# Performance work log

Measured on AMD Instinct MI355X. Metric: run time of the kernel, lower is better.

Reference implementation:

```python
import jax, jax.numpy as jnp
import numpy as np

H, DM, LQ, LK, DK, DV = 16, 1024, 2048, 2048, 64, 64
B = 2

def setup_inputs() -> dict:
    key = jax.random.key(0)
    ks = jax.random.split(key, 12)
    s = 0.02  # init scale for weights
    return {
        "Q": jax.random.normal(ks[0], (B, LQ, DM), jnp.float32),
        "K": jax.random.normal(ks[1], (B, LK, DM), jnp.float32),
        "V": jax.random.normal(ks[2], (B, LK, DM), jnp.float32),
        "mask": jax.random.randint(ks[3], (B, LQ), 0, 2, jnp.int32),
        "W_Q": jax.random.normal(ks[4], (H * DK, DM), jnp.float32) * s,
        "b_Q": jnp.zeros((H * DK,), jnp.float32),
        "W_K": jax.random.normal(ks[5], (H * DK, DM), jnp.float32) * s,
        "b_K": jnp.zeros((H * DK,), jnp.float32),
        "W_V": jax.random.normal(ks[6], (H * DV, DM), jnp.float32) * s,
        "b_V": jnp.zeros((H * DV,), jnp.float32),
        "W_O": jax.random.normal(ks[7], (DM, H * DV), jnp.float32) * s,
        "b_O": jnp.zeros((DM,), jnp.float32),
    }

def reference(Q, K, V, mask, W_Q, b_Q, W_K, b_K, W_V, b_V, W_O, b_O):
    b = Q.shape[0]
    q = (Q @ W_Q.T + b_Q).reshape(b, LQ, H, DK)
    k = (K @ W_K.T + b_K).reshape(b, LK, H, DK)
    v = (V @ W_V.T + b_V).reshape(b, LK, H, DV)
    # scores: [b, h, q, k]
    A = jnp.einsum('bqhd,bkhd->bhqk', q, k) / jnp.sqrt(jnp.float32(DK))
    # mask masks whole QUERY rows; softmax is over the query axis (dim=1 in torch's [B*h, lq, lk])
    A = jnp.where(mask[:, None, :, None] == 0, -jnp.inf, A)
    alpha = jax.nn.softmax(A, axis=2)  # over query axis, per original masked branch
    out = jnp.einsum('bhqk,bkhd->bqhd', alpha, v).reshape(b, LQ, H * DV)
    return out @ W_O.T + b_O + Q  # output proj + residual
```

## Files before the change

### kernel.cpp

```cpp
#include <hip/hip_runtime.h>
#include <hip/hip_bf16.h>
#include <stdint.h>

using frag8 = __attribute__((ext_vector_type(8))) short;
using f32x4 = __attribute__((ext_vector_type(4))) float;

#define MFMA16 __builtin_amdgcn_mfma_f32_16x16x32_bf16

#if __has_builtin(__builtin_amdgcn_exp2f)
#define EXP2F(x) __builtin_amdgcn_exp2f(x)
#else
#define EXP2F(x) __expf((x) * 0.6931471805599453f)
#endif
#if __has_builtin(__builtin_amdgcn_rcpf)
#define RCPF(x) __builtin_amdgcn_rcpf(x)
#else
#define RCPF(x) (1.0f / (x))
#endif

#define SCALE_Q 0.18033688011112042f

__device__ __forceinline__ short f2bf(float f) {
    union { __hip_bfloat16 h; short s; } c;
    c.h = __float2bfloat16(f);
    return c.s;
}
__device__ __forceinline__ float bf2f(short s) {
    union { uint32_t u; float f; } x; x.u = ((uint32_t)(uint16_t)s) << 16;
    return x.f;
}
__device__ __forceinline__ uint32_t pack2bf(float a, float b) {
    float2 t; t.x = a; t.y = b;
    __hip_bfloat162 h = __float22bfloat162_rn(t);
    union { __hip_bfloat162 h; uint32_t u; } c; c.h = h;
    return c.u;
}
__device__ __forceinline__ uint32_t addpk(uint32_t a, uint32_t b) {
    float a0 = bf2f((short)(a & 0xffff)), a1 = bf2f((short)(a >> 16));
    float b0 = bf2f((short)(b & 0xffff)), b1 = bf2f((short)(b >> 16));
    return pack2bf(a0 + b0, a1 + b1);
}
__device__ __forceinline__ frag8 add8(uint4 x, uint4 y) {
    union { uint32_t u[4]; frag8 f; } r;
    r.u[0] = addpk(x.x, y.x); r.u[1] = addpk(x.y, y.y);
    r.u[2] = addpk(x.z, y.z); r.u[3] = addpk(x.w, y.w);
    return r.f;
}

__global__ __launch_bounds__(64) void k_compact(const int* __restrict__ mask,
                                                int* __restrict__ idx,
                                                int* __restrict__ invp,
                                                int* __restrict__ nU) {
    const int b = blockIdx.x, ln = threadIdx.x;
    const int* m = mask + b * 2048;
    int tot = 0;
    for (int c = 0; c < 32; c++)
        tot += __popcll(__ballot(m[c * 64 + ln] != 0));
    int base = 0, mbase = tot;
    for (int c = 0; c < 32; c++) {
        int i = c * 64 + ln;
        int mv = m[i];
        unsigned long long bal = __ballot(mv != 0);
        int rank = __popcll(bal & ((1ull << ln) - 1ull));
        int nb = __popcll(bal);
        int pos = mv ? (base + rank) : (mbase + ln - rank);
        invp[b * 2048 + i] = pos;
        if (mv) idx[b * 2048 + pos] = i;
        base += nb; mbase += 64 - nb;
    }
    if (ln == 0) nU[b] = tot;
}

__global__ __launch_bounds__(256) void k_psum(short* __restrict__ p0,
                                              const short* __restrict__ p1, int n8) {
    int i = blockIdx.x * 256 + threadIdx.x;
    int st = gridDim.x * 256;
    for (; i < n8; i += st) {
        uint4 a = ((const uint4*)p0)[i];
        uint4 b = ((const uint4*)p1)[i];
        frag8 r = add8(a, b);
        ((uint4*)p0)[i] = *(uint4*)&r;
    }
}

__global__ __launch_bounds__(256) void k_maskout(const int* __restrict__ mask,
                                                 const float* __restrict__ bO,
                                                 const float* __restrict__ Qf,
                                                 float* __restrict__ out) {
    int i = blockIdx.x * 256 + threadIdx.x;
    int st = gridDim.x * 256;
    const int total = 4096 * 256;
    for (; i < total; i += st) {
        int row = i >> 8, c4 = i & 255;
        if (mask[row] == 0) {
            float4 q = ((const float4*)Qf)[i];
            float4 bv = ((const float4*)bO)[c4];
            float4 o; o.x = q.x + bv.x; o.y = q.y + bv.y;
            o.z = q.z + bv.z; o.w = q.w + bv.w;
            ((float4*)out)[i] = o;
        }
    }
}

__global__ __launch_bounds__(256) void k_cvt_all(
    const float* __restrict__ s0, const float* __restrict__ s1,
    const float* __restrict__ s2, const float* __restrict__ s3,
    const float* __restrict__ s4, const float* __restrict__ s5,
    const float* __restrict__ s6, const int* __restrict__ invp,
    short* __restrict__ d0, short* __restrict__ d1, short* __restrict__ d2,
    short* __restrict__ d3, short* __restrict__ d4, short* __restrict__ d5,
    short* __restrict__ d6) {
    const int A4 = 1048576, W4 = 262144;
    int i = blockIdx.x * 256 + threadIdx.x;
    int st = gridDim.x * 256;
    const int total = 3 * A4 + 4 * W4;
    for (; i < total; i += st) {
        const float* s; short* d; int j;
        bool permQ = false;
        if (i < A4)            { s = s0; d = d0; j = i; permQ = true; }
        else if (i < 2 * A4)   { s = s1; d = d1; j = i - A4; }
        else if (i < 3 * A4)   { s = s2; d = d2; j = i - 2 * A4; }
        else {
            int t = i - 3 * A4; int seg = t / W4; j = t - seg * W4;
            s = seg == 0 ? s3 : seg == 1 ? s4 : seg == 2 ? s5 : s6;
            d = seg == 0 ? d3 : seg == 1 ? d4 : seg == 2 ? d5 : d6;
        }
        float4 v = reinterpret_cast<const float4*>(s)[j];
        uint2 o;
        o.x = pack2bf(v.x, v.y);
        o.y = pack2bf(v.z, v.w);
        int jd = j;
        if (permQ) {
            int row = j >> 8, c4 = j & 255;
            int nrow = (row & ~2047) + invp[row];
            jd = (nrow << 8) + c4;
        }
        reinterpret_cast<uint2*>(d)[jd] = o;
    }
}

__device__ __forceinline__ void stage64x128(const short* __restrict__ g, int rs,
                                            short* lds, int tid) {
#pragma unroll
    for (int j = 0; j < 2; j++) {
        int chunk = j * 256 + tid;
        int row = chunk >> 3, c = chunk & 7;
        int sc = c ^ (row & 7);
        __builtin_amdgcn_global_load_lds(
            (const __attribute__((address_space(1))) uint32_t*)(g + (size_t)row * rs + sc * 8),
            (__attribute__((address_space(3))) uint32_t*)(lds + (j * 256 + (tid & 192)) * 8),
            16, 0, 0);
    }
}
__device__ __forceinline__ frag8 ldswz(const short* lds, int row, int cc) {
    return *(const frag8*)(lds + row * 64 + ((cc ^ (row & 7)) << 3));
}

__device__ __forceinline__ void stage_gswz(const short* __restrict__ g,
                                           short* lds, int tid) {
#pragma unroll
    for (int j = 0; j < 2; j++) {
        int c = j * 256 + tid;
        int lrow = c >> 3;
        int sc = (c & 7) ^ (lrow & 7);
        int grow = lrow * 2 + (sc >> 2);
        int gcol = (sc & 3) * 8;
        __builtin_amdgcn_global_load_lds(
            (const __attribute__((address_space(1))) uint32_t*)(g + (size_t)grow * 1024 + gcol),
            (__attribute__((address_space(3))) uint32_t*)(lds + (j * 256 + (tid & 192)) * 8),
            16, 0, 0);
    }
}
__device__ __forceinline__ void stage_gswz64(const short* __restrict__ g,
                                             short* lds, int tid) {
    int c = tid;
    int lrow = c >> 3;
    int sc = (c & 7) ^ (lrow & 7);
    int grow = lrow * 2 + (sc >> 2);
    int gcol = (sc & 3) * 8;
    __builtin_amdgcn_global_load_lds(
        (const __attribute__((address_space(1))) uint32_t*)(g + (size_t)grow * 1024 + gcol),
        (__attribute__((address_space(3))) uint32_t*)(lds + (tid & 192) * 8),
        16, 0, 0);
}
__device__ __forceinline__ frag8 ldgswz(const short* lds, int row, int cc) {
    int lrow = row >> 1;
    int s = (((row & 1) << 2) + cc) ^ (lrow & 7);
    return *(const frag8*)(lds + lrow * 64 + s * 8);
}

__global__ __launch_bounds__(256) void k_proj3(
    const short* __restrict__ A0, const short* __restrict__ A1, const short* __restrict__ A2,
    const short* __restrict__ B0, const short* __restrict__ B1, const short* __restrict__ B2,
    const float* __restrict__ bias0, const float* __restrict__ bias1, const float* __restrict__ bias2,
    const int* __restrict__ nU,
    short* __restrict__ dst0, short* __restrict__ dst1, short* __restrict__ dst2) {
    __shared__ short lA[2][4096];
    __shared__ short lB[2][4096];
    const int wg = blockIdx.x;
    const int tmlow = wg & 7, tnb = (wg >> 3) & 7, rest = wg >> 6;
    const int tmh = rest & 3, z = rest >> 2;
    const int tmb = tmlow | (tmh << 3);
    if (z == 0 && (tmb & 15) * 128 >= nU[tmb >> 4]) return;
    const short* A  = z == 0 ? A0 : z == 1 ? A1 : A2;
    const short* Bt = z == 0 ? B0 : z == 1 ? B1 : B2;
    const float* bias = z == 0 ? bias0 : z == 1 ? bias1 : bias2;
    short* dst = z == 0 ? dst0 : z == 1 ? dst1 : dst2;
    const float scale = z == 0 ? SCALE_Q : 1.0f;

    const int tid = threadIdx.x, w = tid >> 6, ln = tid & 63;
    const int wm = w >> 1, wn = w & 1, r16 = ln & 15, g = ln >> 4;
    const int tn = tnb * 128, tm = tmb * 128;
    const short* Ab = A + (size_t)tm * 1024;
    const short* Bb = Bt + (size_t)tn * 1024;

    f32x4 acc[4][4] = {};
    stage_gswz(Ab, &lA[0][0], tid);
    stage_gswz(Bb, &lB[0][0], tid);
    int buf = 0;
    for (int ks = 0; ks < 32; ks++) {
        __syncthreads();
        if (ks + 1 < 32) {
            stage_gswz(Ab + (ks + 1) * 32, &lA[buf ^ 1][0], tid);
            stage_gswz(Bb + (ks + 1) * 32, &lB[buf ^ 1][0], tid);
        }
        frag8 af[4], bg[4];
#pragma unroll
        for (int mf = 0; mf < 4; mf++)
            af[mf] = ldgswz(&lA[buf][0], wm * 64 + mf * 16 + r16, g);
#pragma unroll
        for (int nf = 0; nf < 4; nf++)
            bg[nf] = ldgswz(&lB[buf][0], wn * 64 + nf * 16 + r16, g);
#pragma unroll
        for (int mf = 0; mf < 4; mf++)
#pragma unroll
            for (int nf = 0; nf < 4; nf++)
                acc[mf][nf] = MFMA16(af[mf], bg[nf], acc[mf][nf], 0, 0, 0);
        buf ^= 1;
    }
#pragma unroll
    for (int mf = 0; mf < 4; mf++)
#pragma unroll
        for (int r = 0; r < 4; r++) {
            int m = tm + wm * 64 + mf * 16 + g * 4 + r;
            int b = m >> 11, seq = m & 2047;
#pragma unroll
            for (int nf = 0; nf < 4; nf++) {
                int n = tn + wn * 64 + nf * 16 + r16;
                float val = (acc[mf][nf][r] + bias[n]) * scale;
                int h = n >> 6, d = n & 63;
                dst[((size_t)(b * 16 + h) * 2048 + seq) * 64 + d] = f2bf(val);
            }
        }
}

__global__ __launch_bounds__(256, 3) void k_stats(const short* __restrict__ k_s,
                                                  const short* __restrict__ q_s,
                                                  const int* __restrict__ nU,
                                                  const short* __restrict__ v_s,
                                                  short* __restrict__ vhatT) {
    __shared__ short lQ[2][4096];
    __shared__ float lD[128];
    __shared__ short lT[128 * 70];
    const int wg = blockIdx.x;
    const int x = wg & 7, r2 = wg >> 3;
    const int kt = r2 & 15;
    const int bh = x + 8 * (r2 >> 4);
    const int b = bh >> 4;
    const int n = nU[b], nUr = (n + 63) & ~63;
    const int tid = threadIdx.x, w = tid >> 6, ln = tid & 63;
    const int r16 = ln & 15, g = ln >> 4;
    const int kbase = kt * 128 + w * 32;

    const short* kp = k_s + ((size_t)bh * 2048 + kbase) * 64;
    frag8 kf[2][2];
#pragma unroll
    for (int mfk = 0; mfk < 2; mfk++)
#pragma unroll
        for (int kk = 0; kk < 2; kk++)
            kf[mfk][kk] = *(const frag8*)(kp + (mfk * 16 + r16) * 64 + kk * 32 + g * 8);

    const short* qsp = q_s + (size_t)bh * 2048 * 64;
    float dacc[2][4] = {};
    const f32x4 z4 = {0.f, 0.f, 0.f, 0.f};

    if (nUr > 0) {
        stage64x128(qsp, 64, &lQ[0][0], tid);
        int buf = 0;
        for (int qb = 0; qb < nUr; qb += 64) {
            __syncthreads();
            if (qb + 64 < nUr)
                stage64x128(qsp + (size_t)(qb + 64) * 64, 64, &lQ[buf ^ 1][0], tid);
            const short* Qc = &lQ[buf][0];
#pragma unroll
            for (int nf = 0; nf < 4; nf++) {
                float fm = (qb + nf * 16 + r16 < n) ? 1.0f : 0.0f;
                frag8 bq0 = ldswz(Qc, nf * 16 + r16, g);
                frag8 bq1 = ldswz(Qc, nf * 16 + r16, 4 + g);
#pragma unroll
                for (int mfk = 0; mfk < 2; mfk++) {
                    f32x4 s = MFMA16(kf[mfk][0], bq0, z4, 0, 0, 0);
                    s = MFMA16(kf[mfk][1], bq1, s, 0, 0, 0);
#pragma unroll
                    for (int r = 0; r < 4; r++)
                        dacc[mfk][r] += fm * EXP2F(s[r]);
                }
            }
            buf ^= 1;
        }
    }
#pragma unroll
    for (int mfk = 0; mfk < 2; mfk++)
#pragma unroll
        for (int r = 0; r < 4; r++) {
            float v = dacc[mfk][r];
#pragma unroll
            for (int off = 1; off < 16; off <<= 1)
                v += __shfl_xor(v, off, 16);
            dacc[mfk][r] = v;
        }
    if (r16 == 0) {
#pragma unroll
        for (int mfk = 0; mfk < 2; mfk++)
#pragma unroll
            for (int r = 0; r < 4; r++)
                lD[w * 32 + mfk * 16 + g * 4 + r] = RCPF(dacc[mfk][r]);
    }
    const short* vrow = v_s + ((size_t)bh * 2048 + kt * 128) * 64;
#pragma unroll
    for (int i = 0; i < 8; i++) {
        int idx4 = i * 256 + tid;
        int row = idx4 >> 4, c4 = idx4 & 15;
        uint2 u = *(const uint2*)(vrow + (size_t)row * 64 + c4 * 4);
        *(uint32_t*)&lT[row * 70 + c4 * 4]     = u.x;
        *(uint32_t*)&lT[row * 70 + c4 * 4 + 2] = u.y;
    }
    __syncthreads();
    {
        int d = tid >> 2, kc = tid & 3;
        short* dstp = vhatT + ((size_t)bh * 64 + d) * 2048 + kt * 128 + kc * 32;
        uint32_t wd[16];
#pragma unroll
        for (int j2 = 0; j2 < 16; j2++) {
            int k0 = kc * 32 + j2 * 2;
            float v0 = bf2f(lT[k0 * 70 + d]) * lD[k0];
            float v1 = bf2f(lT[(k0 + 1) * 70 + d]) * lD[k0 + 1];
            wd[j2] = pack2bf(v0, v1);
        }
#pragma unroll
        for (int j4 = 0; j4 < 4; j4++) {
            uint4 o = {wd[j4 * 4], wd[j4 * 4 + 1], wd[j4 * 4 + 2], wd[j4 * 4 + 3]};
            *((uint4*)dstp + j4) = o;
        }
    }
}

__global__ __launch_bounds__(256, 3) void k_apply(const short* __restrict__ q_s,
                                                  const short* __restrict__ k_s,
                                                  const short* __restrict__ vhatT,
                                                  const int* __restrict__ nU,
                                                  short* __restrict__ p0,
                                                  short* __restrict__ p1) {
    __shared__ short lK[2][4096];
    __shared__ short lV[2][4096];
    __shared__ short lP[128 * 64];
    const int wg = blockIdx.x;
    const int x = wg & 7, r2 = wg >> 3;
    const int qt = r2 & 15, y = r2 >> 4;
    const int bhsp = (y << 3) | x;
    const int bh = bhsp >> 1, sp = bhsp & 1;
    const int b = bh >> 4, h = bh & 15;
    const int n = nU[b];
    if (qt * 128 >= n) return;
    const int tid = threadIdx.x, w = tid >> 6, ln = tid & 63;
    const int r16 = ln & 15, g = ln >> 4;

    const short* qp = q_s + ((size_t)bh * 2048 + qt * 128 + w * 32) * 64;
    frag8 qf[2][2];
#pragma unroll
    for (int qi = 0; qi < 2; qi++)
#pragma unroll
        for (int kk = 0; kk < 2; kk++)
            qf[qi][kk] = *(const frag8*)(qp + (qi * 16 + r16) * 64 + kk * 32 + g * 8);

    const short* kp = k_s + ((size_t)bh * 2048 + sp * 1024) * 64;
    const short* vp = vhatT + (size_t)bh * 64 * 2048 + sp * 1024;

    f32x4 oacc[2][4] = {};
    const f32x4 z4 = {0.f, 0.f, 0.f, 0.f};

    stage64x128(kp, 64, &lK[0][0], tid);
    stage64x128(vp, 2048, &lV[0][0], tid);
    int buf = 0;
    for (int kb = 0; kb < 1024; kb += 64) {
        __syncthreads();
        if (kb + 64 < 1024) {
            stage64x128(kp + (size_t)(kb + 64) * 64, 64, &lK[buf ^ 1][0], tid);
            stage64x128(vp + kb + 64, 2048, &lV[buf ^ 1][0], tid);
        }
        const short* Kc = &lK[buf][0];
        const short* Vc = &lV[buf][0];
        frag8 vb[4][2];
#pragma unroll
        for (int nf = 0; nf < 4; nf++)
#pragma unroll
            for (int kk = 0; kk < 2; kk++)
                vb[nf][kk] = ldswz(Vc, nf * 16 + r16, kk * 4 + g);
#pragma unroll
        for (int qi = 0; qi < 2; qi++) {
            const int prow = w * 32 + qi * 16 + r16;
            const int rx = prow & 7;
#pragma unroll
            for (int mf2 = 0; mf2 < 4; mf2++) {
                f32x4 s = z4;
#pragma unroll
                for (int kk = 0; kk < 2; kk++)
                    s = MFMA16(ldswz(Kc, mf2 * 16 + r16, kk * 4 + g), qf[qi][kk], s, 0, 0, 0);
                float e0 = EXP2F(s[0]), e1 = EXP2F(s[1]);
                float e2 = EXP2F(s[2]), e3 = EXP2F(s[3]);
                uint2 pk;
                pk.x = pack2bf(e0, e1);
                pk.y = pack2bf(e2, e3);
                int o = mf2 * 32 + g * 8;
                int addr = prow * 128 + (((o >> 4) ^ rx) << 4) + (o & 15);
                *(uint2*)((char*)lP + addr) = pk;
            }
        }
#pragma unroll
        for (int qi = 0; qi < 2; qi++) {
            const int prow = w * 32 + qi * 16 + r16;
            const int rx = prow & 7;
            frag8 pa[2];
#pragma unroll
            for (int kk = 0; kk < 2; kk++)
                pa[kk] = *(const frag8*)((char*)lP + prow * 128 + (((kk * 4 + g) ^ rx) << 4));
#pragma unroll
            for (int nf = 0; nf < 4; nf++)
#pragma unroll
                for (int kk = 0; kk < 2; kk++)
                    oacc[qi][nf] = MFMA16(pa[kk], vb[nf][kk], oacc[qi][nf], 0, 0, 0);
        }
        buf ^= 1;
    }
    short* op = sp ? p1 : p0;
#pragma unroll
    for (int qi = 0; qi < 2; qi++)
#pragma unroll
        for (int r = 0; r < 4; r++) {
            int lq = qt * 128 + w * 32 + qi * 16 + g * 4 + r;
            if (lq < n) {
#pragma unroll
                for (int nf = 0; nf < 4; nf++) {
                    int d = nf * 16 + r16;
                    op[((size_t)(b * 2048 + lq)) * 1024 + h * 64 + d] = f2bf(oacc[qi][nf][r]);
                }
            }
        }
}

__global__ __launch_bounds__(256) void k_final(const short* __restrict__ A,
                                               const short* __restrict__ Bt,
                                               const float* __restrict__ bias,
                                               const float* __restrict__ Qres,
                                               const int* __restrict__ idx,
                                               const int* __restrict__ nU,
                                               float* __restrict__ out) {
    __shared__ short lA[2][4096];
    __shared__ short lB[2][2048];
    const int wg = blockIdx.x;
    const int x = wg & 7, r2 = wg >> 3;
    const int tnb = r2 & 15, tmh = r2 >> 4;
    const int tmb = x | (tmh << 3);
    const int bb = tmb >> 4;
    const int n = nU[bb];
    if ((tmb & 15) * 128 >= n) return;
    const int tid = threadIdx.x, w = tid >> 6, ln = tid & 63;
    const int wm = w >> 1, wn = w & 1, r16 = ln & 15, g = ln >> 4;
    const int tn = tnb * 64, tm = tmb * 128;
    const short* Ab = A + (size_t)tm * 1024;
    const short* Bb = Bt + (size_t)tn * 1024;

    f32x4 acc[4][2] = {};
    stage_gswz(Ab, &lA[0][0], tid);
    stage_gswz64(Bb, &lB[0][0], tid);
    int buf = 0;
    for (int ks = 0; ks < 32; ks++) {
        __syncthreads();
        if (ks + 1 < 32) {
            stage_gswz(Ab + (ks + 1) * 32, &lA[buf ^ 1][0], tid);
            stage_gswz64(Bb + (ks + 1) * 32, &lB[buf ^ 1][0], tid);
        }
        frag8 af[4], bg[2];
#pragma unroll
        for (int mf = 0; mf < 4; mf++)
            af[mf] = ldgswz(&lA[buf][0], wm * 64 + mf * 16 + r16, g);
#pragma unroll
        for (int nf = 0; nf < 2; nf++)
            bg[nf] = ldgswz(&lB[buf][0], wn * 32 + nf * 16 + r16, g);
#pragma unroll
        for (int mf = 0; mf < 4; mf++)
#pragma unroll
            for (int nf = 0; nf < 2; nf++)
                acc[mf][nf] = MFMA16(af[mf], bg[nf], acc[mf][nf], 0, 0, 0);
        buf ^= 1;
    }
#pragma unroll
    for (int mf = 0; mf < 4; mf++)
#pragma unroll
        for (int r = 0; r < 4; r++) {
            int m = tm + wm * 64 + mf * 16 + g * 4 + r;
            int i = m & 2047;
            if (i < n) {
                int qg = idx[bb * 2048 + i];
                size_t rowo = ((size_t)(bb * 2048 + qg)) * 1024;
#pragma unroll
                for (int nf = 0; nf < 2; nf++) {
                    int nn = tn + wn * 32 + nf * 16 + r16;
                    float val = acc[mf][nf][r] + bias[nn] + Qres[rowo + nn];
                    out[rowo + nn] = val;
                }
            }
        }
}

extern "C" void kernel_launch(void* const* d_in, const int* in_sizes, int n_in,
                              void* d_out, int out_size, void* d_ws, size_t ws_size,
                              hipStream_t stream) {
    (void)in_sizes; (void)n_in; (void)out_size; (void)ws_size;
    const float* Qf  = (const float*)d_in[0];
    const float* Kf  = (const float*)d_in[1];
    const float* Vf  = (const float*)d_in[2];
    const int*   msk = (const int*)d_in[3];
    const float* WQ  = (const float*)d_in[4];
    const float* bQ  = (const float*)d_in[5];
    const float* WK  = (const float*)d_in[6];
    const float* bK  = (const float*)d_in[7];
    const float* WV  = (const float*)d_in[8];
    const float* bV  = (const float*)d_in[9];
    const float* WO  = (const float*)d_in[10];
    const float* bO  = (const float*)d_in[11];
    float* out = (float*)d_out;

    char* p = (char*)d_ws;
    const size_t SZ_ACT = (size_t)4096 * 1024 * 2;
    const size_t SZ_W   = (size_t)1024 * 1024 * 2;
    short* Qb  = (short*)p; p += SZ_ACT;
    short* Kb  = (short*)p; p += SZ_ACT;
    short* Vb  = (short*)p; p += SZ_ACT;
    short* q_s = (short*)p; p += SZ_ACT;
    short* k_s = (short*)p; p += SZ_ACT;
    short* v_s = (short*)p; p += SZ_ACT;
    short* Wqb = (short*)p; p += SZ_W;
    short* Wkb = (short*)p; p += SZ_W;
    short* Wvb = (short*)p; p += SZ_W;
    short* Wob = (short*)p; p += SZ_W;
    int* idx  = (int*)p; p += (size_t)2 * 2048 * 4;
    int* invp = (int*)p; p += (size_t)2 * 2048 * 4;
    int* nU   = (int*)p; p += 256;
    short* vhatT = Qb;
    short* p0    = Kb;
    short* p1    = Vb;

    k_compact<<<2, 64, 0, stream>>>(msk, idx, invp, nU);

    k_cvt_all<<<4096, 256, 0, stream>>>(Qf, Kf, Vf, WQ, WK, WV, WO, invp,
                                        Qb, Kb, Vb, Wqb, Wkb, Wvb, Wob);

    k_proj3<<<768, 256, 0, stream>>>(Qb, Kb, Vb, Wqb, Wkb, Wvb,
                                     bQ, bK, bV, nU, q_s, k_s, v_s);

    k_stats<<<512, 256, 0, stream>>>(k_s, q_s, nU, v_s, vhatT);

    k_apply<<<1024, 256, 0, stream>>>(q_s, k_s, vhatT, nU, p0, p1);

    k_psum<<<2048, 256, 0, stream>>>(p0, p1, 524288);

    k_maskout<<<2048, 256, 0, stream>>>(msk, bO, Qf, out);

    k_final<<<512, 256, 0, stream>>>(p0, Wob, bO, Qf, idx, nU, out);
}
```

Before: 155.3 us.

## Split attention apply across three key chunks and fuse partial-sum with mask output

The apply kernel's key dimension now splits three ways (11/11/10 chunks of 64) instead of two, giving 1536 workgroups rather than 1024 for better CU occupancy and load balance. The partial-sum kernel now adds three bf16 partials, and the masked-row output kernel is folded into it, which removes one launch. The trade-off is an extra partial buffer to write and read (reusing v_s) and more rounding from summing three bf16 partials.

New measurement: 156.9 us. Within noise of the previous version (+1.0%).

```diff
diff --git a/kernel.cpp b/kernel.cpp
--- a/kernel.cpp
+++ b/kernel.cpp
@@ -35,16 +35,11 @@
     union { __hip_bfloat162 h; uint32_t u; } c; c.h = h;
     return c.u;
 }
-__device__ __forceinline__ uint32_t addpk(uint32_t a, uint32_t b) {
+__device__ __forceinline__ uint32_t addpk3(uint32_t a, uint32_t b, uint32_t c) {
     float a0 = bf2f((short)(a & 0xffff)), a1 = bf2f((short)(a >> 16));
     float b0 = bf2f((short)(b & 0xffff)), b1 = bf2f((short)(b >> 16));
-    return pack2bf(a0 + b0, a1 + b1);
-}
-__device__ __forceinline__ frag8 add8(uint4 x, uint4 y) {
-    union { uint32_t u[4]; frag8 f; } r;
-    r.u[0] = addpk(x.x, y.x); r.u[1] = addpk(x.y, y.y);
-    r.u[2] = addpk(x.z, y.z); r.u[3] = addpk(x.w, y.w);
-    return r.f;
+    float c0 = bf2f((short)(c & 0xffff)), c1 = bf2f((short)(c >> 16));
+    return pack2bf(a0 + b0 + c0, a1 + b1 + c1);
 }
 
 __global__ __launch_bounds__(64) void k_compact(const int* __restrict__ mask,
@@ -71,26 +66,27 @@
     if (ln == 0) nU[b] = tot;
 }
 
-__global__ __launch_bounds__(256) void k_psum(short* __restrict__ p0,
-                                              const short* __restrict__ p1, int n8) {
-    int i = blockIdx.x * 256 + threadIdx.x;
+__global__ __launch_bounds__(256) void k_psum3m(short* __restrict__ p0,
+                                                const short* __restrict__ p1,
+                                                const short* __restrict__ p2,
+                                                const int* __restrict__ mask,
+                                                const float* __restrict__ bO,
+                                                const float* __restrict__ Qf,
+                                                float* __restrict__ out) {
+    const int n16 = 524288;
+    int i0 = blockIdx.x * 256 + threadIdx.x;
     int st = gridDim.x * 256;
-    for (; i < n8; i += st) {
+    for (int i = i0; i < n16; i += st) {
         uint4 a = ((const uint4*)p0)[i];
         uint4 b = ((const uint4*)p1)[i];
-        frag8 r = add8(a, b);
-        ((uint4*)p0)[i] = *(uint4*)&r;
-    }
-}
-
-__global__ __launch_bounds__(256) void k_maskout(const int* __restrict__ mask,
-                                                 const float* __restrict__ bO,
-                                                 const float* __restrict__ Qf,
-                                                 float* __restrict__ out) {
-    int i = blockIdx.x * 256 + threadIdx.x;
-    int st = gridDim.x * 256;
+        uint4 c = ((const uint4*)p2)[i];
+        uint4 r;
+        r.x = addpk3(a.x, b.x, c.x); r.y = addpk3(a.y, b.y, c.y);
+        r.z = addpk3(a.z, b.z, c.z); r.w = addpk3(a.w, b.w, c.w);
+        ((uint4*)p0)[i] = r;
+    }
     const int total = 4096 * 256;
-    for (; i < total; i += st) {
+    for (int i = i0; i < total; i += st) {
         int row = i >> 8, c4 = i & 255;
         if (mask[row] == 0) {
             float4 q = ((const float4*)Qf)[i];
@@ -360,18 +356,19 @@
                                                   const short* __restrict__ vhatT,
                                                   const int* __restrict__ nU,
                                                   short* __restrict__ p0,
-                                                  short* __restrict__ p1) {
+                                                  short* __restrict__ p1,
+                                                  short* __restrict__ p2) {
     __shared__ short lK[2][4096];
     __shared__ short lV[2][4096];
     __shared__ short lP[128 * 64];
     const int wg = blockIdx.x;
-    const int x = wg & 7, r2 = wg >> 3;
-    const int qt = r2 & 15, y = r2 >> 4;
-    const int bhsp = (y << 3) | x;
-    const int bh = bhsp >> 1, sp = bhsp & 1;
+    const int x = wg & 7, qt = (wg >> 3) & 15, y = wg >> 7;
+    const int bhsp = y * 8 + x;
+    const int bh = bhsp / 3, sp = bhsp - bh * 3;
     const int b = bh >> 4, h = bh & 15;
     const int n = nU[b];
     if (qt * 128 >= n) return;
+    const int kc0 = sp * 11, nch = (sp == 2) ? 10 : 11;
     const int tid = threadIdx.x, w = tid >> 6, ln = tid & 63;
     const int r16 = ln & 15, g = ln >> 4;
 
@@ -383,8 +380,8 @@
         for (int kk = 0; kk < 2; kk++)
             qf[qi][kk] = *(const frag8*)(qp + (qi * 16 + r16) * 64 + kk * 32 + g * 8);
 
-    const short* kp = k_s + ((size_t)bh * 2048 + sp * 1024) * 64;
-    const short* vp = vhatT + (size_t)bh * 64 * 2048 + sp * 1024;
+    const short* kp = k_s + ((size_t)bh * 2048 + kc0 * 64) * 64;
+    const short* vp = vhatT + (size_t)bh * 64 * 2048 + kc0 * 64;
 
     f32x4 oacc[2][4] = {};
     const f32x4 z4 = {0.f, 0.f, 0.f, 0.f};
@@ -392,11 +389,11 @@
     stage64x128(kp, 64, &lK[0][0], tid);
     stage64x128(vp, 2048, &lV[0][0], tid);
     int buf = 0;
-    for (int kb = 0; kb < 1024; kb += 64) {
+    for (int c = 0; c < nch; c++) {
         __syncthreads();
-        if (kb + 64 < 1024) {
-            stage64x128(kp + (size_t)(kb + 64) * 64, 64, &lK[buf ^ 1][0], tid);
-            stage64x128(vp + kb + 64, 2048, &lV[buf ^ 1][0], tid);
+        if (c + 1 < nch) {
+            stage64x128(kp + (size_t)(c + 1) * 64 * 64, 64, &lK[buf ^ 1][0], tid);
+            stage64x128(vp + (c + 1) * 64, 2048, &lV[buf ^ 1][0], tid);
         }
         const short* Kc = &lK[buf][0];
         const short* Vc = &lV[buf][0];
@@ -442,7 +439,7 @@
         }
         buf ^= 1;
     }
-    short* op = sp ? p1 : p0;
+    short* op = sp == 0 ? p0 : sp == 1 ? p1 : p2;
 #pragma unroll
     for (int qi = 0; qi < 2; qi++)
 #pragma unroll
@@ -560,6 +557,7 @@
     short* vhatT = Qb;
     short* p0    = Kb;
     short* p1    = Vb;
+    short* p2    = v_s;
 
     k_compact<<<2, 64, 0, stream>>>(msk, idx, invp, nU);
 
@@ -571,11 +569,9 @@
 
     k_stats<<<512, 256, 0, stream>>>(k_s, q_s, nU, v_s, vhatT);
 
-    k_apply<<<1024, 256, 0, stream>>>(q_s, k_s, vhatT, nU, p0, p1);
-
-    k_psum<<<2048, 256, 0, stream>>>(p0, p1, 524288);
-
-    k_maskout<<<2048, 256, 0, stream>>>(msk, bO, Qf, out);
+    k_apply<<<1536, 256, 0, stream>>>(q_s, k_s, vhatT, nU, p0, p1, p2);
+
+    k_psum3m<<<2048, 256, 0, stream>>>(p0, p1, p2, msk, bO, Qf, out);
 
     k_final<<<512, 256, 0, stream>>>(p0, Wob, bO, Qf, idx, nU, out);
 }
```
